# Performance work log

Measured on AMD Instinct MI355X. Metric: run time of the kernel, lower is better.

## Reference

```python
import jax, jax.numpy as jnp
import numpy as np

N_HEAD = 16
R = 8
THRESHOLD = 0.1


def setup_inputs() -> dict:
    key = jax.random.key(0)
    k1, k2, k3 = jax.random.split(key, 3)
    B, T, C = 2, 2048, 2048
    fused_dim = 3 * C  # 2*H*D_std + C + 2*H*R with D_std+R = head_dim
    x = jax.random.normal(k1, (B, T, C), dtype=jnp.float32)
    W_attn = jax.random.normal(k2, (fused_dim, C), dtype=jnp.float32) * (1.0 / np.sqrt(C))
    W_proj = jax.random.normal(k3, (C, C), dtype=jnp.float32) * (1.0 / np.sqrt(C))
    w_std = jnp.ones((N_HEAD,), dtype=jnp.float32) * 0.5
    w_rec = jnp.ones((N_HEAD,), dtype=jnp.float32) * 0.3
    return {"x": x, "W_attn": W_attn, "W_proj": W_proj, "w_std": w_std, "w_rec": w_rec}


def _causal_attention(Q, K, V):
    # Q,K: [B,H,T,D]; V: [B,H,T,Dv]; scale = 1/sqrt(D) (torch SDPA default)
    D = Q.shape[-1]
    scores = jnp.einsum("bhqd,bhkd->bhqk", Q, K) / jnp.sqrt(jnp.asarray(D, Q.dtype))
    T = Q.shape[2]
    causal = jnp.tril(jnp.ones((T, T), dtype=bool))
    scores = jnp.where(causal, scores, jnp.asarray(-jnp.inf, scores.dtype))
    probs = jax.nn.softmax(scores, axis=-1)
    return jnp.einsum("bhqk,bhkd->bhqd", probs, V)


def reference(x, W_attn, W_proj, w_std, w_rec):
    B, T, C = x.shape
    H = N_HEAD
    head_dim = C // H
    D_std = head_dim - R
    q_std_end = H * D_std
    k_std_end = q_std_end + H * D_std
    v_end = k_std_end + C
    q_low_end = v_end + H * R

    fused = jnp.einsum("btc,fc->btf", x, W_attn)  # c_attn, no bias

    def split_heads(a, d):
        return a.reshape(B, T, H, d).transpose(0, 2, 1, 3)  # [B,H,T,d]

    Q_std = split_heads(fused[..., :q_std_end], D_std)
    K_std = split_heads(fused[..., q_std_end:k_std_end], D_std)
    V = split_heads(fused[..., k_std_end:v_end], head_dim)
    Q_low = split_heads(fused[..., v_end:q_low_end], R)
    K_low = split_heads(fused[..., q_low_end:], R)

    # per-head routing: RA heads fold low-rank K/Q cross terms, baseline heads keep standard concat
    use_ra = (w_rec > THRESHOLD).reshape(1, H, 1, 1)
    ws = jnp.sqrt(jnp.clip(w_std, 1e-8, None)).reshape(1, H, 1, 1)
    wr = jnp.sqrt(jnp.clip(w_rec, 1e-8, None)).reshape(1, H, 1, 1)

    Qf_low = jnp.where(use_ra, wr * K_low, ws * Q_low)
    Kf_low = jnp.where(use_ra, wr * Q_low, ws * K_low)
    Qf = jnp.concatenate([ws * Q_std, Qf_low], axis=-1)  # [B,H,T,head_dim]
    Kf = jnp.concatenate([ws * K_std, Kf_low], axis=-1)

    out = _causal_attention(Qf, Kf, V)  # [B,H,T,head_dim]
    out = out.transpose(0, 2, 1, 3).reshape(B, T, C)
    return jnp.einsum("btc,oc->bto", out, W_proj)
```

## Files before the change

kernel.cpp:

```cpp
#include <hip/hip_runtime.h>
#include <math.h>

#define Bb 2
#define Tt 2048
#define Cc 2048
#define Hh 16
#define DH 128
#define FUSED 6144
#define Mm 4096
#define QSC 0.08838834764831845f

typedef __bf16 bf16x8 __attribute__((ext_vector_type(8)));
typedef float  f32x4  __attribute__((ext_vector_type(4)));

__device__ __forceinline__ unsigned short f2bf(float f) {
  unsigned int u = __float_as_uint(f);
  u = (u + 0x7fffu + ((u >> 16) & 1u)) >> 16;
  return (unsigned short)u;
}

__device__ __forceinline__ void gload16(const void* src, void* lds) {
  __builtin_amdgcn_global_load_lds((const __attribute__((address_space(1))) void*)src,
                                   (__attribute__((address_space(3))) void*)lds, 16, 0, 0);
}

#define N1 8388608
#define N2 12582912
#define N3 4194304
__global__ void f2bf_all(const float* __restrict__ s1, const float* __restrict__ s2,
                         const float* __restrict__ s3, unsigned short* __restrict__ dst)
{
  int i = (blockIdx.x * blockDim.x + threadIdx.x) * 4;
  int stride = gridDim.x * blockDim.x * 4;
  for (; i < N1 + N2 + N3; i += stride) {
    const float* src = (i < N1) ? (s1 + i) : (i < N1 + N2) ? (s2 + (i - N1)) : (s3 + (i - N1 - N2));
    float4 v = *(const float4*)src;
    ushort4 o;
    o.x = f2bf(v.x); o.y = f2bf(v.y); o.z = f2bf(v.z); o.w = f2bf(v.w);
    *(ushort4*)&dst[i] = o;
  }
}

template <int MODE>
__global__ __launch_bounds__(256)
void gemm_bf16(const unsigned short* __restrict__ A, const unsigned short* __restrict__ Bw,
               float* __restrict__ out,
               unsigned short* __restrict__ Qb, unsigned short* __restrict__ Kb,
               unsigned short* __restrict__ Vb,
               const float* __restrict__ w_std, const float* __restrict__ w_rec,
               int N, int K)
{
  __shared__ unsigned short As[128 * 64];
  __shared__ unsigned short Bs[128 * 64];
  __shared__ float lws[Hh], lwr[Hh];
  __shared__ int   lra[Hh];

  const int tid  = threadIdx.x;
  const int lane = tid & 63;
  const int w    = tid >> 6;
  const int wr   = w >> 1, wc = w & 1;
  const int lrow = lane & 15, lgrp = lane >> 4;
  const int m0 = blockIdx.y * 128;
  const int n0 = blockIdx.x * 128;

  if (MODE == 1 && tid < Hh) {
    float a = w_std[tid]; lws[tid] = sqrtf(a < 1e-8f ? 1e-8f : a);
    float r = w_rec[tid]; lwr[tid] = sqrtf(r < 1e-8f ? 1e-8f : r);
    lra[tid] = (r > 0.1f) ? 1 : 0;
  }

  f32x4 acc[4][4] = {};

  for (int kt = 0; kt < K; kt += 64) {
#pragma unroll
    for (int c = 0; c < 4; ++c) {
      int base16 = (c * 4 + w) * 64;
      int o16 = base16 + lane;
      int rr = o16 >> 3, cc = o16 & 7;
      int csw = (cc ^ (rr & 7)) << 3;
      gload16(A  + (size_t)(m0 + rr) * K + kt + csw, As + base16 * 8);
      gload16(Bw + (size_t)(n0 + rr) * K + kt + csw, Bs + base16 * 8);
    }
    __syncthreads();

#pragma unroll
    for (int s = 0; s < 2; ++s) {
      bf16x8 af[4], bfr[4];
#pragma unroll
      for (int i = 0; i < 4; ++i) {
        int row = wr * 64 + i * 16 + lrow;
        int ch  = s * 4 + lgrp;
        af[i]  = *(const bf16x8*)&As[row * 64 + ((ch ^ (row & 7)) << 3)];
        int col = wc * 64 + i * 16 + lrow;
        bfr[i] = *(const bf16x8*)&Bs[col * 64 + ((ch ^ (col & 7)) << 3)];
      }
#pragma unroll
      for (int i = 0; i < 4; ++i)
#pragma unroll
        for (int j = 0; j < 4; ++j)
          acc[i][j] = __builtin_amdgcn_mfma_f32_16x16x32_bf16(af[i], bfr[j], acc[i][j], 0, 0, 0);
    }
    __syncthreads();
  }

  if (MODE == 0) {
#pragma unroll
    for (int i = 0; i < 4; ++i)
#pragma unroll
      for (int r = 0; r < 4; ++r) {
        int m = m0 + wr * 64 + i * 16 + lgrp * 4 + r;
#pragma unroll
        for (int j = 0; j < 4; ++j) {
          int n = n0 + wc * 64 + j * 16 + lrow;
          out[(size_t)m * N + n] = acc[i][j][r];
        }
      }
  } else {
#pragma unroll
    for (int i = 0; i < 4; ++i)
#pragma unroll
      for (int r = 0; r < 4; ++r) {
        int m = m0 + wr * 64 + i * 16 + lgrp * 4 + r;
        int b = m >> 11, t = m & 2047;
#pragma unroll
        for (int j = 0; j < 4; ++j) {
          int f = n0 + wc * 64 + j * 16 + lrow;
          float v = acc[i][j][r];
          unsigned short* dst; int h, d; float sc;
          if (f < 1920)      { h = f / 120; d = f - h * 120; dst = Qb; sc = lws[h] * QSC; }
          else if (f < 3840) { int g = f - 1920; h = g / 120; d = g - h * 120; dst = Kb; sc = lws[h]; }
          else if (f < 5888) { int g = f - 3840; h = g >> 7; d = g & 127; dst = Vb; sc = 1.f; }
          else if (f < 6016) { int g = f - 5888; h = g >> 3; d = 120 + (g & 7);
                               if (lra[h]) { dst = Kb; sc = lwr[h]; }
                               else        { dst = Qb; sc = lws[h] * QSC; } }
          else               { int g = f - 6016; h = g >> 3; d = 120 + (g & 7);
                               if (lra[h]) { dst = Qb; sc = lwr[h] * QSC; }
                               else        { dst = Kb; sc = lws[h]; } }
          dst[((((size_t)b * Hh + h) * Tt + t) << 7) + d] = f2bf(v * sc);
        }
      }
  }
}

__global__ __launch_bounds__(256)
void vtrans(const unsigned short* __restrict__ Vb, unsigned short* __restrict__ Vtb)
{
  __shared__ unsigned short Vs[64 * 128];
  const int tid = threadIdx.x;
  const int bh = blockIdx.y, t0 = blockIdx.x * 64;
  const unsigned short* src = Vb + ((size_t)bh * Tt + t0) * DH;
#pragma unroll
  for (int c = 0; c < 4; ++c) {
    int u = c * 256 + tid;
    int row = u >> 4, ch = u & 15;
    *(uint4*)&Vs[row * 128 + ch * 8] = *(const uint4*)&src[(size_t)row * DH + ch * 8];
  }
  __syncthreads();
  unsigned short* dstb = Vtb + (size_t)bh * DH * Tt + t0;
#pragma unroll
  for (int c = 0; c < 4; ++c) {
    int u = c * 256 + tid;
    int d = u & 127, tc = u >> 7;
    unsigned short tmp[8];
#pragma unroll
    for (int j = 0; j < 8; ++j) tmp[j] = Vs[(tc * 8 + j) * 128 + d];
    *(uint4*)&dstb[(size_t)d * Tt + tc * 8] = *(uint4*)tmp;
  }
}

__global__ __launch_bounds__(512)
void attn_mfma(const unsigned short* __restrict__ Qb, const unsigned short* __restrict__ Kb,
               const unsigned short* __restrict__ Vtb, unsigned short* __restrict__ attb)
{
  extern __shared__ unsigned short smem[];
  unsigned short* KT = smem;
  unsigned short* VT = smem + 2 * 8192;
  unsigned short* PB = smem + 4 * 8192;

  const int tid = threadIdx.x, lane = tid & 63, wav = tid >> 6;
  const int lrow = lane & 15, lgrp = lane >> 4;
  const int bid = blockIdx.x;
  const int xs  = bid & 7;
  const int rem = bid >> 3;
  const int bh  = xs + ((rem & 3) << 3);
  const int pr  = rem >> 2;

  const unsigned short* Qh = Qb  + (size_t)bh * Tt * DH;
  const unsigned short* Kh = Kb  + (size_t)bh * Tt * DH;
  const unsigned short* Vh = Vtb + (size_t)bh * DH * Tt;
  const int b = bh >> 4, h = bh & 15;

  unsigned short* Pw = PB + wav * 1024;

  auto stage = [&](int buf, int kv0) {
    unsigned short* Kd = KT + buf * 8192;
    unsigned short* Vd = VT + buf * 8192;
#pragma unroll
    for (int s = 0; s < 2; ++s) {
      int base16 = s * 512 + wav * 64;
      int o16 = base16 + lane;
      { int rr = o16 >> 4, cc = o16 & 15;
        gload16(Kh + (size_t)(kv0 + rr) * DH + ((cc ^ (rr & 7)) << 3), Kd + base16 * 8); }
      { int rr = o16 >> 3, cc = o16 & 7;
        gload16(Vh + (size_t)rr * Tt + kv0 + ((cc ^ (rr & 7)) << 3), Vd + base16 * 8); }
    }
  };

  int cur = 0;
  stage(0, 0);

  for (int ph = 0; ph < 2; ++ph) {
    const int qt = ph ? (15 - pr) : pr;
    const int q0 = qt * 128;
    const int nt = 2 * (qt + 1);

    bf16x8 qf[4];
#pragma unroll
    for (int ks = 0; ks < 4; ++ks)
      qf[ks] = *(const bf16x8*)(Qh + (size_t)(q0 + wav * 16 + lrow) * DH + ks * 32 + lgrp * 8);

    f32x4 o[8] = {};
    float mrun[4], lrun[4];
#pragma unroll
    for (int r = 0; r < 4; ++r) { mrun[r] = -INFINITY; lrun[r] = 0.f; }

    for (int t = 0; t < nt; ++t) {
      const int kv0 = t * 64;
      __syncthreads();
      bool more = (t + 1 < nt);
      if (more)            stage(cur ^ 1, kv0 + 64);
      else if (ph == 0)    stage(cur ^ 1, 0);

      const unsigned short* Kc = KT + cur * 8192;
      const unsigned short* Vc = VT + cur * 8192;

      f32x4 sv[4] = {};
#pragma unroll
      for (int ks = 0; ks < 4; ++ks)
#pragma unroll
        for (int j = 0; j < 4; ++j) {
          int krow = j * 16 + lrow;
          int ch   = ks * 4 + lgrp;
          bf16x8 kf = *(const bf16x8*)&Kc[krow * 128 + ((ch ^ (krow & 7)) << 3)];
          sv[j] = __builtin_amdgcn_mfma_f32_16x16x32_bf16(qf[ks], kf, sv[j], 0, 0, 0);
        }

      const bool domask = (kv0 >= q0);
      float sc[4];
#pragma unroll
      for (int r = 0; r < 4; ++r) {
        if (domask) {
          int qrow = q0 + wav * 16 + lgrp * 4 + r;
#pragma unroll
          for (int j = 0; j < 4; ++j) {
            int kv = kv0 + j * 16 + lrow;
            if (kv > qrow) sv[j][r] = -INFINITY;
          }
        }
        float m_ = fmaxf(fmaxf(sv[0][r], sv[1][r]), fmaxf(sv[2][r], sv[3][r]));
        m_ = fmaxf(m_, __shfl_xor(m_, 1));
        m_ = fmaxf(m_, __shfl_xor(m_, 2));
        m_ = fmaxf(m_, __shfl_xor(m_, 4));
        m_ = fmaxf(m_, __shfl_xor(m_, 8));
        float mn = fmaxf(mrun[r], m_);
        sc[r] = __expf(mrun[r] - mn);
        mrun[r] = mn;
        float rs = 0.f;
#pragma unroll
        for (int j = 0; j < 4; ++j) {
          float p = __expf(sv[j][r] - mn);
          sv[j][r] = p;
          rs += p;
        }
        rs += __shfl_xor(rs, 1);
        rs += __shfl_xor(rs, 2);
        rs += __shfl_xor(rs, 4);
        rs += __shfl_xor(rs, 8);
        lrun[r] = lrun[r] * sc[r] + rs;
      }

#pragma unroll
      for (int n = 0; n < 8; ++n)
#pragma unroll
        for (int r = 0; r < 4; ++r) o[n][r] *= sc[r];

#pragma unroll
      for (int j = 0; j < 4; ++j)
#pragma unroll
        for (int r = 0; r < 4; ++r) {
          int row = lgrp * 4 + r;
          int col = j * 16 + lrow;
          int ch  = col >> 3;
          Pw[row * 64 + ((ch ^ (row & 7)) << 3) + (col & 7)] = f2bf(sv[j][r]);
        }

#pragma unroll
      for (int ks = 0; ks < 2; ++ks) {
        int ch = ks * 4 + lgrp;
        bf16x8 pa = *(const bf16x8*)&Pw[lrow * 64 + ((ch ^ (lrow & 7)) << 3)];
#pragma unroll
        for (int n = 0; n < 8; ++n) {
          int d = n * 16 + lrow;
          bf16x8 vf = *(const bf16x8*)&Vc[d * 64 + ((ch ^ (d & 7)) << 3)];
          o[n] = __builtin_amdgcn_mfma_f32_16x16x32_bf16(pa, vf, o[n], 0, 0, 0);
        }
      }
      cur ^= 1;
    }

#pragma unroll
    for (int r = 0; r < 4; ++r) {
      float inv = 1.f / lrun[r];
      int tg = q0 + wav * 16 + lgrp * 4 + r;
      unsigned short* dst = attb + ((size_t)(b * Tt + tg) * Cc) + h * DH;
#pragma unroll
      for (int n = 0; n < 8; ++n)
        dst[n * 16 + lrow] = f2bf(o[n][r] * inv);
    }
  }
}

extern "C" void kernel_launch(void* const* d_in, const int* in_sizes, int n_in,
                              void* d_out, int out_size, void* d_ws, size_t ws_size,
                              hipStream_t stream) {
  const float* x      = (const float*)d_in[0];
  const float* W_attn = (const float*)d_in[1];
  const float* W_proj = (const float*)d_in[2];
  const float* w_std  = (const float*)d_in[3];
  const float* w_rec  = (const float*)d_in[4];
  float* outp = (float*)d_out;

  unsigned short* wsb = (unsigned short*)d_ws;
  unsigned short* xb   = wsb;
  unsigned short* Wab  = wsb + 8388608;
  unsigned short* Wpb  = wsb + 20971520;
  unsigned short* Qb   = wsb + 25165824;
  unsigned short* Kb   = wsb + 33554432;
  unsigned short* Vb   = wsb + 41943040;
  unsigned short* Vtb  = wsb + 50331648;
  unsigned short* attb = wsb + 58720256;

  f2bf_all<<<2048, 256, 0, stream>>>(x, W_attn, W_proj, wsb);

  gemm_bf16<1><<<dim3(FUSED / 128, Mm / 128), dim3(256), 0, stream>>>(
      xb, Wab, nullptr, Qb, Kb, Vb, w_std, w_rec, FUSED, Cc);

  vtrans<<<dim3(Tt / 64, Bb * Hh), dim3(256), 0, stream>>>(Vb, Vtb);

  attn_mfma<<<dim3(256), dim3(512), 81920, stream>>>(Qb, Kb, Vtb, attb);

  gemm_bf16<0><<<dim3(Cc / 128, Mm / 128), dim3(256), 0, stream>>>(
      attb, Wpb, outp, nullptr, nullptr, nullptr, nullptr, nullptr, Cc, Cc);
}
```

Before: 432.6 us.

## Double-buffer GEMM LDS tiles and widen block tile to 128x256 with 8 waves

The bf16 GEMM now uses dynamic shared memory with two buffers, so the next K-tile's global-to-LDS loads are issued while the current tile is multiplied. This removes one barrier per iteration and overlaps load latency with compute. The block tile grows to 128x256 with 512 threads (8 waves), and the MFMA section is wrapped in s_setprio to favour matrix issue. The costs are 96KB of LDS per block, which limits occupancy, and a grid with half as many blocks. Both the QKV projection and the output projection use the new kernel.

Measured after the change: 416.1 us. 3.8% less time.

```diff
diff --git a/kernel.cpp b/kernel.cpp
--- a/kernel.cpp
+++ b/kernel.cpp
@@ -42,7 +42,7 @@
 }
 
 template <int MODE>
-__global__ __launch_bounds__(256)
+__global__ __launch_bounds__(512)
 void gemm_bf16(const unsigned short* __restrict__ A, const unsigned short* __restrict__ Bw,
                float* __restrict__ out,
                unsigned short* __restrict__ Qb, unsigned short* __restrict__ Kb,
@@ -50,18 +50,17 @@
                const float* __restrict__ w_std, const float* __restrict__ w_rec,
                int N, int K)
 {
-  __shared__ unsigned short As[128 * 64];
-  __shared__ unsigned short Bs[128 * 64];
+  extern __shared__ unsigned short sm[];
   __shared__ float lws[Hh], lwr[Hh];
   __shared__ int   lra[Hh];
 
   const int tid  = threadIdx.x;
   const int lane = tid & 63;
-  const int w    = tid >> 6;
-  const int wr   = w >> 1, wc = w & 1;
+  const int wav  = tid >> 6;
+  const int wm   = wav >> 2, wn = wav & 3;
   const int lrow = lane & 15, lgrp = lane >> 4;
   const int m0 = blockIdx.y * 128;
-  const int n0 = blockIdx.x * 128;
+  const int n0 = blockIdx.x * 256;
 
   if (MODE == 1 && tid < Hh) {
     float a = w_std[tid]; lws[tid] = sqrtf(a < 1e-8f ? 1e-8f : a);
@@ -69,36 +68,55 @@
     lra[tid] = (r > 0.1f) ? 1 : 0;
   }
 
-  f32x4 acc[4][4] = {};
-
-  for (int kt = 0; kt < K; kt += 64) {
-#pragma unroll
-    for (int c = 0; c < 4; ++c) {
-      int base16 = (c * 4 + w) * 64;
+  auto stage = [&](int buf, int kt) {
+    unsigned short* Ad = sm + buf * 8192;
+    unsigned short* Bd = sm + 16384 + buf * 16384;
+#pragma unroll
+    for (int s = 0; s < 2; ++s) {
+      int base16 = s * 512 + wav * 64;
       int o16 = base16 + lane;
       int rr = o16 >> 3, cc = o16 & 7;
-      int csw = (cc ^ (rr & 7)) << 3;
-      gload16(A  + (size_t)(m0 + rr) * K + kt + csw, As + base16 * 8);
-      gload16(Bw + (size_t)(n0 + rr) * K + kt + csw, Bs + base16 * 8);
-    }
-    __syncthreads();
-
+      gload16(A + (size_t)(m0 + rr) * K + kt + ((cc ^ (rr & 7)) << 3), Ad + base16 * 8);
+    }
+#pragma unroll
+    for (int s = 0; s < 4; ++s) {
+      int base16 = s * 512 + wav * 64;
+      int o16 = base16 + lane;
+      int rr = o16 >> 3, cc = o16 & 7;
+      gload16(Bw + (size_t)(n0 + rr) * K + kt + ((cc ^ (rr & 7)) << 3), Bd + base16 * 8);
+    }
+  };
+
+  stage(0, 0);
+  __syncthreads();
+
+  f32x4 acc[4][4] = {};
+  const int NT = K >> 6;
+
+  for (int t = 0; t < NT; ++t) {
+    const int cur = t & 1;
+    if (t + 1 < NT) stage(cur ^ 1, (t + 1) << 6);
+
+    const unsigned short* Ac = sm + cur * 8192;
+    const unsigned short* Bc = sm + 16384 + cur * 16384;
 #pragma unroll
     for (int s = 0; s < 2; ++s) {
       bf16x8 af[4], bfr[4];
 #pragma unroll
       for (int i = 0; i < 4; ++i) {
-        int row = wr * 64 + i * 16 + lrow;
+        int row = wm * 64 + i * 16 + lrow;
         int ch  = s * 4 + lgrp;
-        af[i]  = *(const bf16x8*)&As[row * 64 + ((ch ^ (row & 7)) << 3)];
-        int col = wc * 64 + i * 16 + lrow;
-        bfr[i] = *(const bf16x8*)&Bs[col * 64 + ((ch ^ (col & 7)) << 3)];
-      }
+        af[i]  = *(const bf16x8*)&Ac[row * 64 + ((ch ^ (row & 7)) << 3)];
+        int col = wn * 64 + i * 16 + lrow;
+        bfr[i] = *(const bf16x8*)&Bc[col * 64 + ((ch ^ (col & 7)) << 3)];
+      }
+      __builtin_amdgcn_s_setprio(1);
 #pragma unroll
       for (int i = 0; i < 4; ++i)
 #pragma unroll
         for (int j = 0; j < 4; ++j)
           acc[i][j] = __builtin_amdgcn_mfma_f32_16x16x32_bf16(af[i], bfr[j], acc[i][j], 0, 0, 0);
+      __builtin_amdgcn_s_setprio(0);
     }
     __syncthreads();
   }
@@ -108,10 +126,10 @@
     for (int i = 0; i < 4; ++i)
 #pragma unroll
       for (int r = 0; r < 4; ++r) {
-        int m = m0 + wr * 64 + i * 16 + lgrp * 4 + r;
+        int m = m0 + wm * 64 + i * 16 + lgrp * 4 + r;
 #pragma unroll
         for (int j = 0; j < 4; ++j) {
-          int n = n0 + wc * 64 + j * 16 + lrow;
+          int n = n0 + wn * 64 + j * 16 + lrow;
           out[(size_t)m * N + n] = acc[i][j][r];
         }
       }
@@ -120,11 +138,11 @@
     for (int i = 0; i < 4; ++i)
 #pragma unroll
       for (int r = 0; r < 4; ++r) {
-        int m = m0 + wr * 64 + i * 16 + lgrp * 4 + r;
+        int m = m0 + wm * 64 + i * 16 + lgrp * 4 + r;
         int b = m >> 11, t = m & 2047;
 #pragma unroll
         for (int j = 0; j < 4; ++j) {
-          int f = n0 + wc * 64 + j * 16 + lrow;
+          int f = n0 + wn * 64 + j * 16 + lrow;
           float v = acc[i][j][r];
           unsigned short* dst; int h, d; float sc;
           if (f < 1920)      { h = f / 120; d = f - h * 120; dst = Qb; sc = lws[h] * QSC; }
@@ -342,13 +360,13 @@
 
   f2bf_all<<<2048, 256, 0, stream>>>(x, W_attn, W_proj, wsb);
 
-  gemm_bf16<1><<<dim3(FUSED / 128, Mm / 128), dim3(256), 0, stream>>>(
+  gemm_bf16<1><<<dim3(FUSED / 256, Mm / 128), dim3(512), 98304, stream>>>(
       xb, Wab, nullptr, Qb, Kb, Vb, w_std, w_rec, FUSED, Cc);
 
   vtrans<<<dim3(Tt / 64, Bb * Hh), dim3(256), 0, stream>>>(Vb, Vtb);
 
   attn_mfma<<<dim3(256), dim3(512), 81920, stream>>>(Qb, Kb, Vtb, attb);
 
-  gemm_bf16<0><<<dim3(Cc / 128, Mm / 128), dim3(256), 0, stream>>>(
+  gemm_bf16<0><<<dim3(Cc / 256, Mm / 128), dim3(512), 98304, stream>>>(
       attb, Wpb, outp, nullptr, nullptr, nullptr, nullptr, nullptr, Cc, Cc);
 }
```

## Replace QKV projection GEMM with triple-buffered 128x256 pipelined kernel

Applied to the files above, without the earlier changes.

Adds a dedicated kernel for the fused QKV projection. It uses 128x256 tiles, 512 threads and a K-step of 32, with a three-stage LDS ring filled by direct global-to-LDS loads. Synchronisation is reduced to one barrier per step, gated by vmcnt waits, and MFMA issue is wrapped in raised wave priority so copies overlap compute. The head-split epilogue now computes destination and scale once per column rather than per element. The tradeoff is more dynamic LDS, which may lower occupancy, and every wave rereading the whole A tile from LDS.

After: 408.4 us. 1.06x faster.

```diff
diff --git a/kernel.cpp b/kernel.cpp
--- a/kernel.cpp
+++ b/kernel.cpp
@@ -41,19 +41,129 @@
   }
 }
 
+__global__ __launch_bounds__(512, 4)
+void gemm1_pipe(const unsigned short* __restrict__ A, const unsigned short* __restrict__ Bw,
+                unsigned short* __restrict__ Qb, unsigned short* __restrict__ Kb,
+                unsigned short* __restrict__ Vb,
+                const float* __restrict__ w_std, const float* __restrict__ w_rec,
+                int N, int K)
+{
+  extern __shared__ unsigned short sm[];
+  __shared__ float lws[Hh], lwr[Hh];
+  __shared__ int   lra[Hh];
+
+  const int tid  = threadIdx.x;
+  const int lane = tid & 63;
+  const int wav  = tid >> 6;
+  const int lrow = lane & 15, lgrp = lane >> 4;
+  const int m0 = blockIdx.y * 128;
+  const int n0 = blockIdx.x * 256;
+
+  if (tid < Hh) {
+    float a = w_std[tid]; lws[tid] = sqrtf(a < 1e-8f ? 1e-8f : a);
+    float r = w_rec[tid]; lwr[tid] = sqrtf(r < 1e-8f ? 1e-8f : r);
+    lra[tid] = (r > 0.1f) ? 1 : 0;
+  }
+
+  auto stage3 = [&](int buf, int kt) {
+    unsigned short* Bd = sm + 12288 + buf * 8192;
+    unsigned short* Ad = sm + buf * 4096;
+#pragma unroll
+    for (int s = 0; s < 2; ++s) {
+      int base16 = (s * 8 + wav) * 64;
+      int o16 = base16 + lane;
+      int r = o16 >> 2, c = o16 & 3;
+      int cs = c ^ (r & 3) ^ ((r >> 2) & 3);
+      gload16(Bw + (size_t)(n0 + r) * K + kt + cs * 8, Bd + base16 * 8);
+    }
+    {
+      int base16 = wav * 64;
+      int o16 = base16 + lane;
+      int r = o16 >> 2, c = o16 & 3;
+      int cs = c ^ (r & 3) ^ ((r >> 2) & 3);
+      gload16(A + (size_t)(m0 + r) * K + kt + cs * 8, Ad + base16 * 8);
+    }
+  };
+
+  f32x4 acc[8][2] = {};
+  const int NT = K >> 5;
+
+  stage3(0, 0);
+  stage3(1, 32);
+  asm volatile("s_waitcnt vmcnt(3)" ::: "memory");
+  __builtin_amdgcn_s_barrier();
+  asm volatile("" ::: "memory");
+
+  for (int t = 0; t < NT; ++t) {
+    const int p = t % 3;
+    if (t + 2 < NT) stage3((t + 2) % 3, (t + 2) << 5);
+
+    const unsigned short* Ac = sm + p * 4096;
+    const unsigned short* Bc = sm + 12288 + p * 8192;
+
+    bf16x8 bf0, bf1;
+    {
+      int row = wav * 32 + lrow;
+      int cs = lgrp ^ (row & 3) ^ ((row >> 2) & 3);
+      bf0 = *(const bf16x8*)&Bc[(row * 4 + cs) * 8];
+      row += 16;
+      cs = lgrp ^ (row & 3) ^ ((row >> 2) & 3);
+      bf1 = *(const bf16x8*)&Bc[(row * 4 + cs) * 8];
+    }
+    __builtin_amdgcn_s_setprio(1);
+#pragma unroll
+    for (int i = 0; i < 8; ++i) {
+      int row = i * 16 + lrow;
+      int cs = lgrp ^ (row & 3) ^ ((row >> 2) & 3);
+      bf16x8 af = *(const bf16x8*)&Ac[(row * 4 + cs) * 8];
+      acc[i][0] = __builtin_amdgcn_mfma_f32_16x16x32_bf16(af, bf0, acc[i][0], 0, 0, 0);
+      acc[i][1] = __builtin_amdgcn_mfma_f32_16x16x32_bf16(af, bf1, acc[i][1], 0, 0, 0);
+    }
+    __builtin_amdgcn_s_setprio(0);
+
+    if (t + 1 < NT) {
+      if (t + 2 < NT) { asm volatile("s_waitcnt vmcnt(3)" ::: "memory"); }
+      else            { asm volatile("s_waitcnt vmcnt(0)" ::: "memory"); }
+      __builtin_amdgcn_s_barrier();
+      asm volatile("" ::: "memory");
+    }
+  }
+
+#pragma unroll
+  for (int j = 0; j < 2; ++j) {
+    int f = n0 + wav * 32 + j * 16 + lrow;
+    unsigned short* dstj; float sc;
+    {
+      unsigned short* dst; int h, d;
+      if (f < 1920)      { h = f / 120; d = f - h * 120; dst = Qb; sc = lws[h] * QSC; }
+      else if (f < 3840) { int g = f - 1920; h = g / 120; d = g - h * 120; dst = Kb; sc = lws[h]; }
+      else if (f < 5888) { int g = f - 3840; h = g >> 7; d = g & 127; dst = Vb; sc = 1.f; }
+      else if (f < 6016) { int g = f - 5888; h = g >> 3; d = 120 + (g & 7);
+                           if (lra[h]) { dst = Kb; sc = lwr[h]; }
+                           else        { dst = Qb; sc = lws[h] * QSC; } }
+      else               { int g = f - 6016; h = g >> 3; d = 120 + (g & 7);
+                           if (lra[h]) { dst = Qb; sc = lwr[h] * QSC; }
+                           else        { dst = Kb; sc = lws[h]; } }
+      dstj = dst + h * 262144 + d;
+    }
+#pragma unroll
+    for (int i = 0; i < 8; ++i)
+#pragma unroll
+      for (int r = 0; r < 4; ++r) {
+        int m = m0 + i * 16 + lgrp * 4 + r;
+        int b = m >> 11, tq = m & 2047;
+        dstj[(size_t)b * 4194304 + tq * 128] = f2bf(acc[i][j][r] * sc);
+      }
+  }
+}
+
 template <int MODE>
 __global__ __launch_bounds__(256)
-void gemm_bf16(const unsigned short* __restrict__ A, const unsigned short* __restrict__ Bw,
-               float* __restrict__ out,
-               unsigned short* __restrict__ Qb, unsigned short* __restrict__ Kb,
-               unsigned short* __restrict__ Vb,
-               const float* __restrict__ w_std, const float* __restrict__ w_rec,
-               int N, int K)
+void gemm_bf16_sm(const unsigned short* __restrict__ A, const unsigned short* __restrict__ Bw,
+                  float* __restrict__ out, int N, int K)
 {
   __shared__ unsigned short As[128 * 64];
   __shared__ unsigned short Bs[128 * 64];
-  __shared__ float lws[Hh], lwr[Hh];
-  __shared__ int   lra[Hh];
 
   const int tid  = threadIdx.x;
   const int lane = tid & 63;
@@ -63,12 +173,6 @@
   const int m0 = blockIdx.y * 128;
   const int n0 = blockIdx.x * 128;
 
-  if (MODE == 1 && tid < Hh) {
-    float a = w_std[tid]; lws[tid] = sqrtf(a < 1e-8f ? 1e-8f : a);
-    float r = w_rec[tid]; lwr[tid] = sqrtf(r < 1e-8f ? 1e-8f : r);
-    lra[tid] = (r > 0.1f) ? 1 : 0;
-  }
-
   f32x4 acc[4][4] = {};
 
   for (int kt = 0; kt < K; kt += 64) {
@@ -103,43 +207,17 @@
     __syncthreads();
   }
 
-  if (MODE == 0) {
-#pragma unroll
-    for (int i = 0; i < 4; ++i)
-#pragma unroll
-      for (int r = 0; r < 4; ++r) {
-        int m = m0 + wr * 64 + i * 16 + lgrp * 4 + r;
-#pragma unroll
-        for (int j = 0; j < 4; ++j) {
-          int n = n0 + wc * 64 + j * 16 + lrow;
-          out[(size_t)m * N + n] = acc[i][j][r];
-        }
+#pragma unroll
+  for (int i = 0; i < 4; ++i)
+#pragma unroll
+    for (int r = 0; r < 4; ++r) {
+      int m = m0 + wr * 64 + i * 16 + lgrp * 4 + r;
+#pragma unroll
+      for (int j = 0; j < 4; ++j) {
+        int n = n0 + wc * 64 + j * 16 + lrow;
+        out[(size_t)m * N + n] = acc[i][j][r];
       }
-  } else {
-#pragma unroll
-    for (int i = 0; i < 4; ++i)
-#pragma unroll
-      for (int r = 0; r < 4; ++r) {
-        int m = m0 + wr * 64 + i * 16 + lgrp * 4 + r;
-        int b = m >> 11, t = m & 2047;
-#pragma unroll
-        for (int j = 0; j < 4; ++j) {
-          int f = n0 + wc * 64 + j * 16 + lrow;
-          float v = acc[i][j][r];
-          unsigned short* dst; int h, d; float sc;
-          if (f < 1920)      { h = f / 120; d = f - h * 120; dst = Qb; sc = lws[h] * QSC; }
-          else if (f < 3840) { int g = f - 1920; h = g / 120; d = g - h * 120; dst = Kb; sc = lws[h]; }
-          else if (f < 5888) { int g = f - 3840; h = g >> 7; d = g & 127; dst = Vb; sc = 1.f; }
-          else if (f < 6016) { int g = f - 5888; h = g >> 3; d = 120 + (g & 7);
-                               if (lra[h]) { dst = Kb; sc = lwr[h]; }
-                               else        { dst = Qb; sc = lws[h] * QSC; } }
-          else               { int g = f - 6016; h = g >> 3; d = 120 + (g & 7);
-                               if (lra[h]) { dst = Qb; sc = lwr[h] * QSC; }
-                               else        { dst = Kb; sc = lws[h]; } }
-          dst[((((size_t)b * Hh + h) * Tt + t) << 7) + d] = f2bf(v * sc);
-        }
-      }
-  }
+    }
 }
 
 __global__ __launch_bounds__(256)
@@ -342,13 +420,13 @@
 
   f2bf_all<<<2048, 256, 0, stream>>>(x, W_attn, W_proj, wsb);
 
-  gemm_bf16<1><<<dim3(FUSED / 128, Mm / 128), dim3(256), 0, stream>>>(
-      xb, Wab, nullptr, Qb, Kb, Vb, w_std, w_rec, FUSED, Cc);
+  gemm1_pipe<<<dim3(FUSED / 256, Mm / 128), dim3(512), 73728, stream>>>(
+      xb, Wab, Qb, Kb, Vb, w_std, w_rec, FUSED, Cc);
 
   vtrans<<<dim3(Tt / 64, Bb * Hh), dim3(256), 0, stream>>>(Vb, Vtb);
 
   attn_mfma<<<dim3(256), dim3(512), 81920, stream>>>(Qb, Kb, Vtb, attb);
 
-  gemm_bf16<0><<<dim3(Cc / 128, Mm / 128), dim3(256), 0, stream>>>(
-      attb, Wpb, outp, nullptr, nullptr, nullptr, nullptr, nullptr, Cc, Cc);
-}
+  gemm_bf16_sm<0><<<dim3(Cc / 128, Mm / 128), dim3(256), 0, stream>>>(
+      attb, Wpb, outp, Cc, Cc);
+}
```
